# Optimization experiments

Hardware: AMD Instinct MI355X
Metric: run time of the kernel (lower is better)

Reference implementation:

```python
import jax, jax.numpy as jnp
import numpy as np

N_NODES = 100000
N_EDGES = 400000
DIM = 3
HID = 32


def _glorot(key, shape):
    fan_in, fan_out = shape[0], shape[1]
    lim = np.sqrt(6.0 / (fan_in + fan_out))
    return jax.random.uniform(key, shape, jnp.float32, -lim, lim)


def setup_inputs() -> dict:
    key = jax.random.key(0)
    ks = jax.random.split(key, 12)
    x = jax.random.normal(ks[0], (N_NODES, DIM), jnp.float32)
    edge_index = jax.random.randint(ks[1], (2, N_EDGES), 0, N_NODES, jnp.int64)
    edge_attr = jax.random.normal(ks[2], (N_EDGES, DIM), jnp.float32)
    params = {
        # conv1: NNConv(3 -> 32), edge nn = Linear(3, 3*32)
        'Wn1': _glorot(ks[3], (DIM, DIM * HID)), 'bn1': jnp.zeros((DIM * HID,), jnp.float32),
        'root1': _glorot(ks[4], (DIM, HID)), 'b1': jnp.zeros((HID,), jnp.float32),
        # conv2: NNConv(32 -> 32), edge nn = Linear(3, 32*32)
        'Wn2': _glorot(ks[5], (DIM, HID * HID)), 'bn2': jnp.zeros((HID * HID,), jnp.float32),
        'root2': _glorot(ks[6], (HID, HID)), 'b2': jnp.zeros((HID,), jnp.float32),
        # fc layers
        'Wf1': _glorot(ks[7], (HID, HID)), 'bf1': jnp.zeros((HID,), jnp.float32),
        'Wf2': _glorot(ks[8], (HID, 1)), 'bf2': jnp.zeros((1,), jnp.float32),
    }
    return {'x': x, 'edge_index': edge_index, 'edge_attr': edge_attr, **params}


def _nnconv(x, src, dst, edge_attr, Wn, bn, root, b, in_c, out_c):
    # per-edge weight matrix from edge MLP: [E, in_c, out_c]
    We = (edge_attr @ Wn + bn).reshape(-1, in_c, out_c)
    # gather source features, per-edge matmul, scatter-add to destinations
    msg = jnp.einsum('ei,eio->eo', x[src], We)  # [E, out_c]
    agg = jax.ops.segment_sum(msg, dst, num_segments=x.shape[0])  # [N, out_c]
    return agg + x @ root + b


def reference(x, edge_index, edge_attr, Wn1, bn1, root1, b1, Wn2, bn2, root2, b2, Wf1, bf1, Wf2, bf2):
    src, dst = edge_index[0], edge_index[1]
    h = jax.nn.relu(_nnconv(x, src, dst, edge_attr, Wn1, bn1, root1, b1, DIM, HID))
    h = jax.nn.relu(_nnconv(h, src, dst, edge_attr, Wn2, bn2, root2, b2, HID, HID))
    h = jax.nn.relu(h @ Wf1 + bf1)
    return h @ Wf2 + bf2  # [N, 1]
```

## Files before the change

kernel.cpp:

```cpp
#include <hip/hip_runtime.h>

#define N_NODES 100000
#define N_EDGES 400000
#define SCAN_BLOCKS ((N_NODES + 255) / 256)

__global__ __launch_bounds__(256) void hist_kernel(const int* __restrict__ ei,
                                                   int* __restrict__ deg) {
    int e = blockIdx.x * 256 + threadIdx.x;
    if (e < N_EDGES) atomicAdd(&deg[ei[N_EDGES + e]], 1);
}

__global__ __launch_bounds__(256) void scanA_kernel(const int* __restrict__ deg,
                                                    int* __restrict__ rowptr,
                                                    int* __restrict__ psum) {
    __shared__ int sm[256];
    int i = blockIdx.x * 256 + threadIdx.x;
    int v = (i < N_NODES) ? deg[i] : 0;
    sm[threadIdx.x] = v;
    __syncthreads();
    #pragma unroll
    for (int off = 1; off < 256; off <<= 1) {
        int t = (threadIdx.x >= off) ? sm[threadIdx.x - off] : 0;
        __syncthreads();
        sm[threadIdx.x] += t;
        __syncthreads();
    }
    if (i < N_NODES) rowptr[i] = sm[threadIdx.x] - v;
    if (threadIdx.x == 255) psum[blockIdx.x] = sm[255];
}

__global__ __launch_bounds__(256) void scanBC_kernel(const int* __restrict__ psum,
                                                     int* __restrict__ rowptr,
                                                     int* __restrict__ cursor) {
    __shared__ int sm[8];
    int bid = blockIdx.x, tid = threadIdx.x;
    int acc = 0;
    for (int t = tid; t < bid; t += 256) acc += psum[t];
    #pragma unroll
    for (int off = 32; off; off >>= 1) acc += __shfl_down(acc, off, 64);
    if ((tid & 63) == 0) sm[tid >> 6] = acc;
    __syncthreads();
    int base = sm[0] + sm[1] + sm[2] + sm[3];
    int i = bid * 256 + tid;
    if (i < N_NODES) {
        int r = rowptr[i] + base;
        rowptr[i] = r;
        cursor[i] = r;
    }
    if (i == 0) rowptr[N_NODES] = N_EDGES;
}

__global__ __launch_bounds__(256) void scatter_kernel(const int* __restrict__ ei,
                                                      const float* __restrict__ ea,
                                                      const float* __restrict__ x,
                                                      int* __restrict__ cursor,
                                                      float4* __restrict__ edataA,
                                                      float4* __restrict__ edataB) {
    int e = blockIdx.x * 256 + threadIdx.x;
    if (e >= N_EDGES) return;
    int s = ei[e], d = ei[N_EDGES + e];
    int pos = atomicAdd(&cursor[d], 1);
    edataA[pos] = make_float4(ea[e*3], ea[e*3+1], ea[e*3+2], __int_as_float(s));
    edataB[pos] = make_float4(x[s*3], x[s*3+1], x[s*3+2], 0.f);
}

__global__ __launch_bounds__(256) void conv1_kernel(const int* __restrict__ rowptr,
                                                    const float4* __restrict__ edataA,
                                                    const float4* __restrict__ edataB,
                                                    const float* __restrict__ x,
                                                    const float* __restrict__ Wn1,
                                                    const float* __restrict__ bn1,
                                                    const float* __restrict__ root1,
                                                    const float* __restrict__ b1,
                                                    float* __restrict__ h1) {
    int gid = blockIdx.x * 256 + threadIdx.x;
    int n = gid >> 5, o = gid & 31;
    if (n >= N_NODES) return;
    float W[3][3], bb[3];
    #pragma unroll
    for (int d2 = 0; d2 < 3; ++d2)
        #pragma unroll
        for (int d = 0; d < 3; ++d) W[d2][d] = Wn1[d2*96 + d*32 + o];
    #pragma unroll
    for (int d = 0; d < 3; ++d) bb[d] = bn1[d*32 + o];

    int j0 = rowptr[n], j1 = rowptr[n + 1];
    float acc0 = 0.f, acc1 = 0.f;
    int j = j0;
    for (; j + 2 <= j1; j += 2) {
        float4 eA0 = edataA[j],   eB0 = edataB[j];
        float4 eA1 = edataA[j+1], eB1 = edataB[j+1];
        float wd0 = fmaf(eA0.x, W[0][0], fmaf(eA0.y, W[1][0], fmaf(eA0.z, W[2][0], bb[0])));
        float wd1 = fmaf(eA0.x, W[0][1], fmaf(eA0.y, W[1][1], fmaf(eA0.z, W[2][1], bb[1])));
        float wd2 = fmaf(eA0.x, W[0][2], fmaf(eA0.y, W[1][2], fmaf(eA0.z, W[2][2], bb[2])));
        acc0 += fmaf(eB0.x, wd0, fmaf(eB0.y, wd1, eB0.z * wd2));
        float ud0 = fmaf(eA1.x, W[0][0], fmaf(eA1.y, W[1][0], fmaf(eA1.z, W[2][0], bb[0])));
        float ud1 = fmaf(eA1.x, W[0][1], fmaf(eA1.y, W[1][1], fmaf(eA1.z, W[2][1], bb[1])));
        float ud2 = fmaf(eA1.x, W[0][2], fmaf(eA1.y, W[1][2], fmaf(eA1.z, W[2][2], bb[2])));
        acc1 += fmaf(eB1.x, ud0, fmaf(eB1.y, ud1, eB1.z * ud2));
    }
    if (j < j1) {
        float4 eA0 = edataA[j], eB0 = edataB[j];
        float wd0 = fmaf(eA0.x, W[0][0], fmaf(eA0.y, W[1][0], fmaf(eA0.z, W[2][0], bb[0])));
        float wd1 = fmaf(eA0.x, W[0][1], fmaf(eA0.y, W[1][1], fmaf(eA0.z, W[2][1], bb[1])));
        float wd2 = fmaf(eA0.x, W[0][2], fmaf(eA0.y, W[1][2], fmaf(eA0.z, W[2][2], bb[2])));
        acc0 += fmaf(eB0.x, wd0, fmaf(eB0.y, wd1, eB0.z * wd2));
    }
    float v = acc0 + acc1 + b1[o];
    v = fmaf(x[n*3],   root1[o],      v);
    v = fmaf(x[n*3+1], root1[32 + o], v);
    v = fmaf(x[n*3+2], root1[64 + o], v);
    h1[(size_t)n*32 + o] = fmaxf(v, 0.f);
}

__global__ __launch_bounds__(256) void prep2_kernel(const float* __restrict__ h1,
                                                    const float* __restrict__ Wn2,
                                                    const float* __restrict__ bn2,
                                                    float4* __restrict__ G2) {
    int o = threadIdx.x & 31;
    float w0[32], w1[32], w2[32], w3[32];
    #pragma unroll
    for (int i = 0; i < 32; ++i) {
        w0[i] = Wn2[         i*32 + o];
        w1[i] = Wn2[1024 +   i*32 + o];
        w2[i] = Wn2[2048 +   i*32 + o];
        w3[i] = bn2[         i*32 + o];
    }
    int g = (blockIdx.x * 256 + threadIdx.x) >> 5;
    int gstep = (gridDim.x * 256) >> 5;
    for (int n = g; n < N_NODES; n += gstep) {
        const float* __restrict__ hr = h1 + (size_t)n * 32;
        float g0 = 0.f, g1 = 0.f, g2 = 0.f, g3 = 0.f;
        #pragma unroll
        for (int i = 0; i < 32; ++i) {
            float hi = hr[i];
            g0 = fmaf(hi, w0[i], g0);
            g1 = fmaf(hi, w1[i], g1);
            g2 = fmaf(hi, w2[i], g2);
            g3 = fmaf(hi, w3[i], g3);
        }
        G2[(size_t)n*32 + o] = make_float4(g0, g1, g2, g3);
    }
}

__global__ __launch_bounds__(256) void conv2_kernel(const int* __restrict__ rowptr,
                                                    const float4* __restrict__ edataA,
                                                    const float4* __restrict__ G2,
                                                    const float* __restrict__ h1,
                                                    const float* __restrict__ root2,
                                                    const float* __restrict__ b2,
                                                    const float* __restrict__ Wf1,
                                                    const float* __restrict__ bf1,
                                                    const float* __restrict__ Wf2,
                                                    const float* __restrict__ bf2,
                                                    float* __restrict__ out) {
    int gid = blockIdx.x * 256 + threadIdx.x;
    int n = gid >> 5, o = gid & 31;
    if (n >= N_NODES) return;
    int j0 = rowptr[n], j1 = rowptr[n + 1];
    float a0 = 0.f, a1 = 0.f, a2 = 0.f, a3v = 0.f;
    int j = j0;
    for (; j + 4 <= j1; j += 4) {
        float4 e0 = edataA[j],   e1 = edataA[j+1];
        float4 e2 = edataA[j+2], e3 = edataA[j+3];
        float4 g0 = G2[(size_t)__float_as_int(e0.w)*32 + o];
        float4 g1 = G2[(size_t)__float_as_int(e1.w)*32 + o];
        float4 g2 = G2[(size_t)__float_as_int(e2.w)*32 + o];
        float4 g3 = G2[(size_t)__float_as_int(e3.w)*32 + o];
        a0 += fmaf(e0.x, g0.x, fmaf(e0.y, g0.y, fmaf(e0.z, g0.z, g0.w)));
        a1 += fmaf(e1.x, g1.x, fmaf(e1.y, g1.y, fmaf(e1.z, g1.z, g1.w)));
        a2 += fmaf(e2.x, g2.x, fmaf(e2.y, g2.y, fmaf(e2.z, g2.z, g2.w)));
        a3v += fmaf(e3.x, g3.x, fmaf(e3.y, g3.y, fmaf(e3.z, g3.z, g3.w)));
    }
    for (; j < j1; ++j) {
        float4 e0 = edataA[j];
        float4 g0 = G2[(size_t)__float_as_int(e0.w)*32 + o];
        a0 += fmaf(e0.x, g0.x, fmaf(e0.y, g0.y, fmaf(e0.z, g0.z, g0.w)));
    }
    float acc = (a0 + a1) + (a2 + a3v);

    const float* __restrict__ hr = h1 + (size_t)n * 32;
    float v = acc + b2[o];
    #pragma unroll
    for (int i = 0; i < 32; ++i) v = fmaf(hr[i], root2[i*32 + o], v);
    float h2 = fmaxf(v, 0.f);

    float a3 = bf1[o];
    #pragma unroll
    for (int i = 0; i < 32; ++i) a3 = fmaf(__shfl(h2, i, 32), Wf1[i*32 + o], a3);
    float h3 = fmaxf(a3, 0.f);

    float p = h3 * Wf2[o];
    #pragma unroll
    for (int off = 16; off; off >>= 1) p += __shfl_down(p, off, 32);
    if (o == 0) out[n] = p + bf2[0];
}

extern "C" void kernel_launch(void* const* d_in, const int* in_sizes, int n_in,
                              void* d_out, int out_size, void* d_ws, size_t ws_size,
                              hipStream_t stream) {
    const float* x     = (const float*)d_in[0];
    const int*   ei    = (const int*)  d_in[1];
    const float* ea    = (const float*)d_in[2];
    const float* Wn1   = (const float*)d_in[3];
    const float* bn1   = (const float*)d_in[4];
    const float* root1 = (const float*)d_in[5];
    const float* b1    = (const float*)d_in[6];
    const float* Wn2   = (const float*)d_in[7];
    const float* bn2   = (const float*)d_in[8];
    const float* root2 = (const float*)d_in[9];
    const float* b2    = (const float*)d_in[10];
    const float* Wf1   = (const float*)d_in[11];
    const float* bf1   = (const float*)d_in[12];
    const float* Wf2   = (const float*)d_in[13];
    const float* bf2   = (const float*)d_in[14];
    float* out = (float*)d_out;

    float*  h1     = (float*)d_ws;
    float4* G2     = (float4*)(h1 + (size_t)N_NODES*32);
    float4* edataA = G2 + (size_t)N_NODES*32;
    float4* edataB = edataA + N_EDGES;
    int*    deg    = (int*)(edataB + N_EDGES);
    int*    rowptr = deg + N_NODES;
    int*    cursor = rowptr + N_NODES + 1;
    int*    psum   = cursor + N_NODES;

    hipMemsetAsync(deg, 0, N_NODES * sizeof(int), stream);

    int eb = (N_EDGES + 255) / 256;
    int nb32 = (N_NODES * 32 + 255) / 256;

    hist_kernel   <<<eb, 256, 0, stream>>>(ei, deg);
    scanA_kernel  <<<SCAN_BLOCKS, 256, 0, stream>>>(deg, rowptr, psum);
    scanBC_kernel <<<SCAN_BLOCKS, 256, 0, stream>>>(psum, rowptr, cursor);
    scatter_kernel<<<eb, 256, 0, stream>>>(ei, ea, x, cursor, edataA, edataB);
    conv1_kernel  <<<nb32, 256, 0, stream>>>(rowptr, edataA, edataB, x, Wn1, bn1, root1, b1, h1);
    prep2_kernel  <<<1536, 256, 0, stream>>>(h1, Wn2, bn2, G2);
    conv2_kernel  <<<nb32, 256, 0, stream>>>(rowptr, edataA, G2, h1, root2, b2,
                                             Wf1, bf1, Wf2, bf2, out);
}
```

Before: 163.9 us.

## Split edges across two half-wavefronts, store G2 in fp16, move FC head to separate kernel

conv1 and conv2 now give each node a full 64-lane wavefront, with the two 32-lane halves taking alternate edges and combining their sums with a shuffle. The precomputed G2 table is stored as packed half2 instead of float4, halving the bytes moved by the random gathers in conv2. The FC head moves out of conv2 into a new per-node-per-thread kernel, which requires writing an extra h2 buffer. The fp16 storage adds rounding error, and the new kernel adds a launch plus an h2 write and read.

Result: slower. 190.2 us (+16.0%).

```diff
diff --git a/kernel.cpp b/kernel.cpp
--- a/kernel.cpp
+++ b/kernel.cpp
@@ -1,4 +1,5 @@
 #include <hip/hip_runtime.h>
+#include <hip/hip_fp16.h>
 
 #define N_NODES 100000
 #define N_EDGES 400000
@@ -73,8 +74,9 @@
                                                     const float* __restrict__ root1,
                                                     const float* __restrict__ b1,
                                                     float* __restrict__ h1) {
-    int gid = blockIdx.x * 256 + threadIdx.x;
-    int n = gid >> 5, o = gid & 31;
+    int n = (blockIdx.x * 256 + threadIdx.x) >> 6;
+    int lane = threadIdx.x & 63;
+    int j2 = lane >> 5, o = lane & 31;
     if (n >= N_NODES) return;
     float W[3][3], bb[3];
     #pragma unroll
@@ -85,38 +87,28 @@
     for (int d = 0; d < 3; ++d) bb[d] = bn1[d*32 + o];
 
     int j0 = rowptr[n], j1 = rowptr[n + 1];
-    float acc0 = 0.f, acc1 = 0.f;
-    int j = j0;
-    for (; j + 2 <= j1; j += 2) {
-        float4 eA0 = edataA[j],   eB0 = edataB[j];
-        float4 eA1 = edataA[j+1], eB1 = edataB[j+1];
-        float wd0 = fmaf(eA0.x, W[0][0], fmaf(eA0.y, W[1][0], fmaf(eA0.z, W[2][0], bb[0])));
-        float wd1 = fmaf(eA0.x, W[0][1], fmaf(eA0.y, W[1][1], fmaf(eA0.z, W[2][1], bb[1])));
-        float wd2 = fmaf(eA0.x, W[0][2], fmaf(eA0.y, W[1][2], fmaf(eA0.z, W[2][2], bb[2])));
-        acc0 += fmaf(eB0.x, wd0, fmaf(eB0.y, wd1, eB0.z * wd2));
-        float ud0 = fmaf(eA1.x, W[0][0], fmaf(eA1.y, W[1][0], fmaf(eA1.z, W[2][0], bb[0])));
-        float ud1 = fmaf(eA1.x, W[0][1], fmaf(eA1.y, W[1][1], fmaf(eA1.z, W[2][1], bb[1])));
-        float ud2 = fmaf(eA1.x, W[0][2], fmaf(eA1.y, W[1][2], fmaf(eA1.z, W[2][2], bb[2])));
-        acc1 += fmaf(eB1.x, ud0, fmaf(eB1.y, ud1, eB1.z * ud2));
-    }
-    if (j < j1) {
-        float4 eA0 = edataA[j], eB0 = edataB[j];
-        float wd0 = fmaf(eA0.x, W[0][0], fmaf(eA0.y, W[1][0], fmaf(eA0.z, W[2][0], bb[0])));
-        float wd1 = fmaf(eA0.x, W[0][1], fmaf(eA0.y, W[1][1], fmaf(eA0.z, W[2][1], bb[1])));
-        float wd2 = fmaf(eA0.x, W[0][2], fmaf(eA0.y, W[1][2], fmaf(eA0.z, W[2][2], bb[2])));
-        acc0 += fmaf(eB0.x, wd0, fmaf(eB0.y, wd1, eB0.z * wd2));
-    }
-    float v = acc0 + acc1 + b1[o];
-    v = fmaf(x[n*3],   root1[o],      v);
-    v = fmaf(x[n*3+1], root1[32 + o], v);
-    v = fmaf(x[n*3+2], root1[64 + o], v);
-    h1[(size_t)n*32 + o] = fmaxf(v, 0.f);
+    float acc = 0.f;
+    for (int j = j0 + j2; j < j1; j += 2) {
+        float4 eA = edataA[j], eB = edataB[j];
+        float wd0 = fmaf(eA.x, W[0][0], fmaf(eA.y, W[1][0], fmaf(eA.z, W[2][0], bb[0])));
+        float wd1 = fmaf(eA.x, W[0][1], fmaf(eA.y, W[1][1], fmaf(eA.z, W[2][1], bb[1])));
+        float wd2 = fmaf(eA.x, W[0][2], fmaf(eA.y, W[1][2], fmaf(eA.z, W[2][2], bb[2])));
+        acc += fmaf(eB.x, wd0, fmaf(eB.y, wd1, eB.z * wd2));
+    }
+    acc += __shfl_xor(acc, 32);
+    if (j2 == 0) {
+        float v = acc + b1[o];
+        v = fmaf(x[n*3],   root1[o],      v);
+        v = fmaf(x[n*3+1], root1[32 + o], v);
+        v = fmaf(x[n*3+2], root1[64 + o], v);
+        h1[(size_t)n*32 + o] = fmaxf(v, 0.f);
+    }
 }
 
 __global__ __launch_bounds__(256) void prep2_kernel(const float* __restrict__ h1,
                                                     const float* __restrict__ Wn2,
                                                     const float* __restrict__ bn2,
-                                                    float4* __restrict__ G2) {
+                                                    uint2* __restrict__ G2h) {
     int o = threadIdx.x & 31;
     float w0[32], w1[32], w2[32], w3[32];
     #pragma unroll
@@ -139,61 +131,71 @@
             g2 = fmaf(hi, w2[i], g2);
             g3 = fmaf(hi, w3[i], g3);
         }
-        G2[(size_t)n*32 + o] = make_float4(g0, g1, g2, g3);
+        __half2 ab = __floats2half2_rn(g0, g1);
+        __half2 cd = __floats2half2_rn(g2, g3);
+        uint2 p;
+        p.x = *(const unsigned int*)&ab;
+        p.y = *(const unsigned int*)&cd;
+        G2h[(size_t)n*32 + o] = p;
     }
 }
 
 __global__ __launch_bounds__(256) void conv2_kernel(const int* __restrict__ rowptr,
                                                     const float4* __restrict__ edataA,
-                                                    const float4* __restrict__ G2,
+                                                    const uint2* __restrict__ G2h,
                                                     const float* __restrict__ h1,
                                                     const float* __restrict__ root2,
                                                     const float* __restrict__ b2,
-                                                    const float* __restrict__ Wf1,
-                                                    const float* __restrict__ bf1,
-                                                    const float* __restrict__ Wf2,
-                                                    const float* __restrict__ bf2,
-                                                    float* __restrict__ out) {
-    int gid = blockIdx.x * 256 + threadIdx.x;
-    int n = gid >> 5, o = gid & 31;
+                                                    float* __restrict__ h2out) {
+    int n = (blockIdx.x * 256 + threadIdx.x) >> 6;
+    int lane = threadIdx.x & 63;
+    int j2 = lane >> 5, o = lane & 31;
     if (n >= N_NODES) return;
     int j0 = rowptr[n], j1 = rowptr[n + 1];
-    float a0 = 0.f, a1 = 0.f, a2 = 0.f, a3v = 0.f;
-    int j = j0;
-    for (; j + 4 <= j1; j += 4) {
-        float4 e0 = edataA[j],   e1 = edataA[j+1];
-        float4 e2 = edataA[j+2], e3 = edataA[j+3];
-        float4 g0 = G2[(size_t)__float_as_int(e0.w)*32 + o];
-        float4 g1 = G2[(size_t)__float_as_int(e1.w)*32 + o];
-        float4 g2 = G2[(size_t)__float_as_int(e2.w)*32 + o];
-        float4 g3 = G2[(size_t)__float_as_int(e3.w)*32 + o];
-        a0 += fmaf(e0.x, g0.x, fmaf(e0.y, g0.y, fmaf(e0.z, g0.z, g0.w)));
-        a1 += fmaf(e1.x, g1.x, fmaf(e1.y, g1.y, fmaf(e1.z, g1.z, g1.w)));
-        a2 += fmaf(e2.x, g2.x, fmaf(e2.y, g2.y, fmaf(e2.z, g2.z, g2.w)));
-        a3v += fmaf(e3.x, g3.x, fmaf(e3.y, g3.y, fmaf(e3.z, g3.z, g3.w)));
-    }
-    for (; j < j1; ++j) {
-        float4 e0 = edataA[j];
-        float4 g0 = G2[(size_t)__float_as_int(e0.w)*32 + o];
-        a0 += fmaf(e0.x, g0.x, fmaf(e0.y, g0.y, fmaf(e0.z, g0.z, g0.w)));
-    }
-    float acc = (a0 + a1) + (a2 + a3v);
-
-    const float* __restrict__ hr = h1 + (size_t)n * 32;
-    float v = acc + b2[o];
-    #pragma unroll
-    for (int i = 0; i < 32; ++i) v = fmaf(hr[i], root2[i*32 + o], v);
-    float h2 = fmaxf(v, 0.f);
-
-    float a3 = bf1[o];
-    #pragma unroll
-    for (int i = 0; i < 32; ++i) a3 = fmaf(__shfl(h2, i, 32), Wf1[i*32 + o], a3);
-    float h3 = fmaxf(a3, 0.f);
-
-    float p = h3 * Wf2[o];
-    #pragma unroll
-    for (int off = 16; off; off >>= 1) p += __shfl_down(p, off, 32);
-    if (o == 0) out[n] = p + bf2[0];
+    float acc = 0.f;
+    for (int j = j0 + j2; j < j1; j += 2) {
+        float4 e = edataA[j];
+        uint2 p = G2h[(size_t)__float_as_int(e.w)*32 + o];
+        __half2 ab = *(const __half2*)&p.x;
+        __half2 cd = *(const __half2*)&p.y;
+        float2 f01 = __half22float2(ab);
+        float2 f23 = __half22float2(cd);
+        acc += fmaf(e.x, f01.x, fmaf(e.y, f01.y, fmaf(e.z, f23.x, f23.y)));
+    }
+    acc += __shfl_xor(acc, 32);
+    if (j2 == 0) {
+        float v = acc + b2[o];
+        const float* __restrict__ hr = h1 + (size_t)n * 32;
+        #pragma unroll
+        for (int i = 0; i < 32; ++i) v = fmaf(hr[i], root2[i*32 + o], v);
+        h2out[(size_t)n*32 + o] = fmaxf(v, 0.f);
+    }
+}
+
+__global__ __launch_bounds__(256) void fc_kernel(const float* __restrict__ h2,
+                                                 const float* __restrict__ Wf1,
+                                                 const float* __restrict__ bf1,
+                                                 const float* __restrict__ Wf2,
+                                                 const float* __restrict__ bf2,
+                                                 float* __restrict__ out) {
+    int n = blockIdx.x * 256 + threadIdx.x;
+    if (n >= N_NODES) return;
+    float hr[32];
+    const float4* hv = (const float4*)(h2 + (size_t)n * 32);
+    #pragma unroll
+    for (int j4 = 0; j4 < 8; ++j4) {
+        float4 t = hv[j4];
+        hr[j4*4+0] = t.x; hr[j4*4+1] = t.y; hr[j4*4+2] = t.z; hr[j4*4+3] = t.w;
+    }
+    float acc2 = bf2[0];
+    #pragma unroll
+    for (int j = 0; j < 32; ++j) {
+        float a = bf1[j];
+        #pragma unroll
+        for (int i = 0; i < 32; ++i) a = fmaf(hr[i], Wf1[i*32 + j], a);
+        acc2 = fmaf(fmaxf(a, 0.f), Wf2[j], acc2);
+    }
+    out[n] = acc2;
 }
 
 extern "C" void kernel_launch(void* const* d_in, const int* in_sizes, int n_in,
@@ -217,8 +219,9 @@
     float* out = (float*)d_out;
 
     float*  h1     = (float*)d_ws;
-    float4* G2     = (float4*)(h1 + (size_t)N_NODES*32);
-    float4* edataA = G2 + (size_t)N_NODES*32;
+    float*  h2     = h1 + (size_t)N_NODES*32;
+    uint2*  G2h    = (uint2*)(h2 + (size_t)N_NODES*32);
+    float4* edataA = (float4*)(G2h + (size_t)N_NODES*32);
     float4* edataB = edataA + N_EDGES;
     int*    deg    = (int*)(edataB + N_EDGES);
     int*    rowptr = deg + N_NODES;
@@ -227,15 +230,16 @@
 
     hipMemsetAsync(deg, 0, N_NODES * sizeof(int), stream);
 
-    int eb = (N_EDGES + 255) / 256;
-    int nb32 = (N_NODES * 32 + 255) / 256;
+    int eb   = (N_EDGES + 255) / 256;
+    int nb   = (N_NODES + 255) / 256;
+    int nb64 = (N_NODES * 64 + 255) / 256;
 
     hist_kernel   <<<eb, 256, 0, stream>>>(ei, deg);
     scanA_kernel  <<<SCAN_BLOCKS, 256, 0, stream>>>(deg, rowptr, psum);
     scanBC_kernel <<<SCAN_BLOCKS, 256, 0, stream>>>(psum, rowptr, cursor);
     scatter_kernel<<<eb, 256, 0, stream>>>(ei, ea, x, cursor, edataA, edataB);
-    conv1_kernel  <<<nb32, 256, 0, stream>>>(rowptr, edataA, edataB, x, Wn1, bn1, root1, b1, h1);
-    prep2_kernel  <<<1536, 256, 0, stream>>>(h1, Wn2, bn2, G2);
-    conv2_kernel  <<<nb32, 256, 0, stream>>>(rowptr, edataA, G2, h1, root2, b2,
-                                             Wf1, bf1, Wf2, bf2, out);
-}
+    conv1_kernel  <<<nb64, 256, 0, stream>>>(rowptr, edataA, edataB, x, Wn1, bn1, root1, b1, h1);
+    prep2_kernel  <<<1536, 256, 0, stream>>>(h1, Wn2, bn2, G2h);
+    conv2_kernel  <<<nb64, 256, 0, stream>>>(rowptr, edataA, G2h, h1, root2, b2, h2);
+    fc_kernel     <<<nb, 256, 0, stream>>>(h2, Wf1, bf1, Wf2, bf2, out);
+}
```

## Split conv2 into edge aggregation kernel and per-node thread dense epilogue

Applied to the files above, without the earlier changes.

Splits the fused conv2 kernel in two. The first kernel only aggregates edge messages into a new h2pre buffer, with its unroll cut from 4 to 2. A separate node2 kernel, one thread per node, then applies the root transform, ReLU and both fc layers using register arrays and uniform weight loads, instead of 32 lanes with shuffles. This adds a 12.8MB round trip through h2pre and an extra launch, and the per-thread 32x32 matmuls create heavy register pressure.

New measurement: 157.0 us. 1.04x faster.

```diff
diff --git a/kernel.cpp b/kernel.cpp
--- a/kernel.cpp
+++ b/kernel.cpp
@@ -146,6 +146,29 @@
 __global__ __launch_bounds__(256) void conv2_kernel(const int* __restrict__ rowptr,
                                                     const float4* __restrict__ edataA,
                                                     const float4* __restrict__ G2,
+                                                    float* __restrict__ h2pre) {
+    int gid = blockIdx.x * 256 + threadIdx.x;
+    int n = gid >> 5, o = gid & 31;
+    if (n >= N_NODES) return;
+    int j0 = rowptr[n], j1 = rowptr[n + 1];
+    float a0 = 0.f, a1 = 0.f;
+    int j = j0;
+    for (; j + 2 <= j1; j += 2) {
+        float4 e0 = edataA[j], e1 = edataA[j+1];
+        float4 g0 = G2[(size_t)__float_as_int(e0.w)*32 + o];
+        float4 g1 = G2[(size_t)__float_as_int(e1.w)*32 + o];
+        a0 += fmaf(e0.x, g0.x, fmaf(e0.y, g0.y, fmaf(e0.z, g0.z, g0.w)));
+        a1 += fmaf(e1.x, g1.x, fmaf(e1.y, g1.y, fmaf(e1.z, g1.z, g1.w)));
+    }
+    if (j < j1) {
+        float4 e0 = edataA[j];
+        float4 g0 = G2[(size_t)__float_as_int(e0.w)*32 + o];
+        a0 += fmaf(e0.x, g0.x, fmaf(e0.y, g0.y, fmaf(e0.z, g0.z, g0.w)));
+    }
+    h2pre[(size_t)n*32 + o] = a0 + a1;
+}
+
+__global__ __launch_bounds__(256) void node2_kernel(const float* __restrict__ h2pre,
                                                     const float* __restrict__ h1,
                                                     const float* __restrict__ root2,
                                                     const float* __restrict__ b2,
@@ -154,46 +177,39 @@
                                                     const float* __restrict__ Wf2,
                                                     const float* __restrict__ bf2,
                                                     float* __restrict__ out) {
-    int gid = blockIdx.x * 256 + threadIdx.x;
-    int n = gid >> 5, o = gid & 31;
+    int n = blockIdx.x * 256 + threadIdx.x;
     if (n >= N_NODES) return;
-    int j0 = rowptr[n], j1 = rowptr[n + 1];
-    float a0 = 0.f, a1 = 0.f, a2 = 0.f, a3v = 0.f;
-    int j = j0;
-    for (; j + 4 <= j1; j += 4) {
-        float4 e0 = edataA[j],   e1 = edataA[j+1];
-        float4 e2 = edataA[j+2], e3 = edataA[j+3];
-        float4 g0 = G2[(size_t)__float_as_int(e0.w)*32 + o];
-        float4 g1 = G2[(size_t)__float_as_int(e1.w)*32 + o];
-        float4 g2 = G2[(size_t)__float_as_int(e2.w)*32 + o];
-        float4 g3 = G2[(size_t)__float_as_int(e3.w)*32 + o];
-        a0 += fmaf(e0.x, g0.x, fmaf(e0.y, g0.y, fmaf(e0.z, g0.z, g0.w)));
-        a1 += fmaf(e1.x, g1.x, fmaf(e1.y, g1.y, fmaf(e1.z, g1.z, g1.w)));
-        a2 += fmaf(e2.x, g2.x, fmaf(e2.y, g2.y, fmaf(e2.z, g2.z, g2.w)));
-        a3v += fmaf(e3.x, g3.x, fmaf(e3.y, g3.y, fmaf(e3.z, g3.z, g3.w)));
-    }
-    for (; j < j1; ++j) {
-        float4 e0 = edataA[j];
-        float4 g0 = G2[(size_t)__float_as_int(e0.w)*32 + o];
-        a0 += fmaf(e0.x, g0.x, fmaf(e0.y, g0.y, fmaf(e0.z, g0.z, g0.w)));
-    }
-    float acc = (a0 + a1) + (a2 + a3v);
-
-    const float* __restrict__ hr = h1 + (size_t)n * 32;
-    float v = acc + b2[o];
-    #pragma unroll
-    for (int i = 0; i < 32; ++i) v = fmaf(hr[i], root2[i*32 + o], v);
-    float h2 = fmaxf(v, 0.f);
-
-    float a3 = bf1[o];
-    #pragma unroll
-    for (int i = 0; i < 32; ++i) a3 = fmaf(__shfl(h2, i, 32), Wf1[i*32 + o], a3);
-    float h3 = fmaxf(a3, 0.f);
-
-    float p = h3 * Wf2[o];
-    #pragma unroll
-    for (int off = 16; off; off >>= 1) p += __shfl_down(p, off, 32);
-    if (o == 0) out[n] = p + bf2[0];
+    float hr[32];
+    const float4* hv = (const float4*)(h1 + (size_t)n * 32);
+    #pragma unroll
+    for (int j4 = 0; j4 < 8; ++j4) {
+        float4 t = hv[j4];
+        hr[j4*4+0] = t.x; hr[j4*4+1] = t.y; hr[j4*4+2] = t.z; hr[j4*4+3] = t.w;
+    }
+    const float4* av = (const float4*)(h2pre + (size_t)n * 32);
+    float h2[32];
+    #pragma unroll
+    for (int j4 = 0; j4 < 8; ++j4) {
+        float4 a = av[j4];
+        #pragma unroll
+        for (int k = 0; k < 4; ++k) {
+            int j = j4*4 + k;
+            float acc = (&a.x)[k] + b2[j];
+            #pragma unroll
+            for (int i = 0; i < 32; ++i)
+                acc = fmaf(hr[i], root2[i*32 + j], acc);
+            h2[j] = fmaxf(acc, 0.f);
+        }
+    }
+    float acc2 = bf2[0];
+    #pragma unroll
+    for (int j = 0; j < 32; ++j) {
+        float a = bf1[j];
+        #pragma unroll
+        for (int i = 0; i < 32; ++i) a = fmaf(h2[i], Wf1[i*32 + j], a);
+        acc2 = fmaf(fmaxf(a, 0.f), Wf2[j], acc2);
+    }
+    out[n] = acc2;
 }
 
 extern "C" void kernel_launch(void* const* d_in, const int* in_sizes, int n_in,
@@ -217,7 +233,8 @@
     float* out = (float*)d_out;
 
     float*  h1     = (float*)d_ws;
-    float4* G2     = (float4*)(h1 + (size_t)N_NODES*32);
+    float*  h2pre  = h1 + (size_t)N_NODES*32;
+    float4* G2     = (float4*)(h2pre + (size_t)N_NODES*32);
     float4* edataA = G2 + (size_t)N_NODES*32;
     float4* edataB = edataA + N_EDGES;
     int*    deg    = (int*)(edataB + N_EDGES);
@@ -227,7 +244,8 @@
 
     hipMemsetAsync(deg, 0, N_NODES * sizeof(int), stream);
 
-    int eb = (N_EDGES + 255) / 256;
+    int eb   = (N_EDGES + 255) / 256;
+    int nb   = (N_NODES + 255) / 256;
     int nb32 = (N_NODES * 32 + 255) / 256;
 
     hist_kernel   <<<eb, 256, 0, stream>>>(ei, deg);
@@ -236,6 +254,6 @@
     scatter_kernel<<<eb, 256, 0, stream>>>(ei, ea, x, cursor, edataA, edataB);
     conv1_kernel  <<<nb32, 256, 0, stream>>>(rowptr, edataA, edataB, x, Wn1, bn1, root1, b1, h1);
     prep2_kernel  <<<1536, 256, 0, stream>>>(h1, Wn2, bn2, G2);
-    conv2_kernel  <<<nb32, 256, 0, stream>>>(rowptr, edataA, G2, h1, root2, b2,
-                                             Wf1, bf1, Wf2, bf2, out);
-}
+    conv2_kernel  <<<nb32, 256, 0, stream>>>(rowptr, edataA, G2, h2pre);
+    node2_kernel  <<<nb, 256, 0, stream>>>(h2pre, h1, root2, b2, Wf1, bf1, Wf2, bf2, out);
+}
```
